# Kernel tuning notes

Hardware: AMD Instinct MI355X
Metric: run time of the kernel (lower is better)

Reference implementation:

```python
import jax, jax.numpy as jnp
import numpy as np

T = 256        # timesteps
N = 100000     # nodes
E = 8192       # edges per timestep
MU_PLUS = 0.1
MU_MINUS = 0.05
RHO = 16.0
CLIP_LO = 1e-5
CLIP_HI = 1.0 - 1e-5


def setup_inputs() -> dict:
    key = jax.random.key(0)
    k1, k2, k3, k4, k5, k6 = jax.random.split(key, 6)
    logit_X0 = jax.random.normal(k1, (N,), dtype=jnp.float32)
    theta = jax.random.normal(k2, (2,), dtype=jnp.float32)
    u = jax.random.randint(k3, (T, E), 0, N)
    v = jax.random.randint(k4, (T, E), 0, N)
    s_plus = jax.random.uniform(k5, (T, E), dtype=jnp.float32)
    s_minus = jax.random.uniform(k6, (T, E), dtype=jnp.float32)
    return {"logit_X0": logit_X0, "theta": theta, "u": u, "v": v,
            "s_plus": s_plus, "s_minus": s_minus}


def _diffuse(X0, u, v, s_plus, s_minus):
    # Equivalent of the dense-materialized row/col sums:
    # update[i] = mu * sum over edges (u,v,w): +w*(X[v]-X[u]) at u, -w*(X[v]-X[u]) at v
    def step(x, edge):
        ut, vt, sp, sm = edge
        d = x[vt] - x[ut]                       # [E]
        def agg(w):
            wd = w * d
            return jnp.zeros_like(x).at[ut].add(wd).at[vt].add(-wd)
        xn = jnp.clip(x + MU_PLUS * agg(sp) - MU_MINUS * agg(sm), CLIP_LO, CLIP_HI)
        return xn, xn
    _, Xs = jax.lax.scan(step, X0, (u[:-1], v[:-1], s_plus[:-1], s_minus[:-1]))
    return jnp.concatenate([X0[None], Xs], axis=0)  # [T, N]


def _kappa(eps, diff, rho):
    # kappa_from_epsilon: acceptance prob of bounded-confidence interaction
    return jax.nn.sigmoid(rho * (eps - jnp.abs(diff)))


def reference(logit_X0, theta, u, v, s_plus, s_minus):
    epsilon_plus = jax.nn.sigmoid(theta[0]) / 2.0
    epsilon_minus = 0.5 + jax.nn.sigmoid(theta[1]) / 2.0
    X0 = jax.nn.sigmoid(logit_X0)
    X = _diffuse(X0, u, v, s_plus, s_minus)            # [T, N]
    Xu = jnp.take_along_axis(X, u, axis=1)             # [T, E]
    Xv = jnp.take_along_axis(X, v, axis=1)             # [T, E]
    diff_X = (Xu - Xv).reshape(-1)                     # [T*E]
    kappa_plus = _kappa(epsilon_plus, diff_X, RHO)
    kappa_minus = _kappa(epsilon_minus, diff_X, -RHO)
    return X, kappa_plus, kappa_minus
```

## Files before the change

### kernel.cpp

```cpp
#include <hip/hip_runtime.h>

#define TSTEPS 256
#define NNODE  100000
#define NEDGE  8192

constexpr float MU_P  = 0.1f;
constexpr float MU_M  = 0.05f;
constexpr float RHO_  = 16.0f;
constexpr float CLO   = 1e-5f;
constexpr float CHI   = 1.0f - 1e-5f;
constexpr float SCALE = 1048576.0f;
constexpr float INVSC = 1.0f / 1048576.0f;

#define SENT32 0xFFFFFFFFu

typedef unsigned long long u64;

__device__ __forceinline__ float sigm(float x) {
  return 1.0f / (1.0f + __expf(-x));
}
__device__ __forceinline__ float x0_of(const float* logit, int n) {
  return fminf(fmaxf(sigm(logit[n]), CLO), CHI);
}
__device__ __forceinline__ int edge_at(const int* __restrict__ arr, int idx,
                                       int is64) {
  if (is64) return (int)((const long long*)arr)[idx];
  return arr[idx];
}

__device__ __forceinline__ u64 pload(const u64* p) {
  return __hip_atomic_load(p, __ATOMIC_RELAXED, __HIP_MEMORY_SCOPE_WORKGROUP);
}
__device__ __forceinline__ void pstore(u64* p, u64 v) {
  __hip_atomic_store(p, v, __ATOMIC_RELAXED, __HIP_MEMORY_SCOPE_WORKGROUP);
}

__device__ __forceinline__ float lazy2(const u64* xs64,
                                       const unsigned* __restrict__ dprev,
                                       int n, unsigned ttag) {
  const u64 a = pload(&xs64[n]);
  const int acc = (int)dprev[n];
  const unsigned tag = (unsigned)(a >> 32);
  const float pv = __uint_as_float((unsigned)a);
  const float cu = fminf(fmaxf(pv + (float)acc * INVSC, CLO), CHI);
  return (tag == ttag) ? pv : cu;
}

__global__ void k_init(const float* __restrict__ logit,
                       const int* __restrict__ u, const int* __restrict__ v,
                       u64* __restrict__ xs64,
                       unsigned* __restrict__ d0, unsigned* __restrict__ d1,
                       unsigned* __restrict__ d2,
                       unsigned* __restrict__ dflags,
                       float* __restrict__ outX) {
  const int i = blockIdx.x * blockDim.x + threadIdx.x;
  const int stride = gridDim.x * blockDim.x;

  if (i == 0) {
    const unsigned* a = (const unsigned*)u;
    const unsigned* b = (const unsigned*)v;
    bool i64 = true;
    for (int k = 1; k < 128; k += 2) i64 = i64 && (a[k] == 0u) && (b[k] == 0u);
    dflags[0] = i64 ? 1u : 0u;
  }

  for (int n = i; n < NNODE; n += stride) {
    xs64[n] = (u64)__float_as_uint(x0_of(logit, n));
    d0[n] = 0u;
    d1[n] = 0u;
    d2[n] = 0u;
    outX[n] = sigm(logit[n]);
  }
  unsigned* outX32 = (unsigned*)outX;
  const int total = TSTEPS * NNODE;
  for (int w = NNODE + i; w < total; w += stride) outX32[w] = SENT32;
}

__global__ void k_prep(const int* __restrict__ u, const int* __restrict__ v,
                       const float* __restrict__ sp, const float* __restrict__ sm,
                       int* __restrict__ uv32u, int* __restrict__ uv32v,
                       float* __restrict__ wsc,
                       const unsigned* __restrict__ dflags) {
  const int g = blockIdx.x * blockDim.x + threadIdx.x;
  if (g >= TSTEPS * NEDGE) return;
  const int is64 = (int)dflags[0];
  uv32u[g] = edge_at(u, g, is64);
  uv32v[g] = edge_at(v, g, is64);
  wsc[g] = (MU_P * sp[g] - MU_M * sm[g]) * SCALE;
}

__global__ __launch_bounds__(256) void k_step(
    const int* __restrict__ uv32u, const int* __restrict__ uv32v,
    const float* __restrict__ wsc,
    u64* __restrict__ xs64,
    unsigned* __restrict__ dcur, const unsigned* __restrict__ dprev,
    unsigned* __restrict__ dzero,
    float* __restrict__ cvals, int t) {
  const int bid = blockIdx.x;
  const int tid = threadIdx.x;
  const unsigned ttag = (unsigned)t;

  if (bid < 32) {
    if (t < TSTEPS - 1) {
      const int i = bid * 256 + tid;
      const int e = t * NEDGE + i;
      const int un = uv32u[e];
      const int vn = uv32v[e];
      const float w = wsc[e];
      const float xu = lazy2(xs64, dprev, un, ttag);
      const float xv = lazy2(xs64, dprev, vn, ttag);
      const int iv = __float2int_rn(w * (xv - xu));
      atomicAdd(&dcur[un], (unsigned)iv);
      atomicAdd(&dcur[vn], (unsigned)(-iv));
    }
  } else if (bid < 96) {
    if (t >= 1) {
      const int j = (bid - 32) * 256 + tid;
      const int e2 = (t - 1) * NEDGE + (j < NEDGE ? j : j - NEDGE);
      const int node = (j < NEDGE) ? uv32u[e2] : uv32v[e2];
      const float val = lazy2(xs64, dprev, node, ttag);
      pstore(&xs64[node], ((u64)ttag << 32) | (u64)__float_as_uint(val));
      cvals[(size_t)(t - 1) * (2 * NEDGE) + j] = val;
    }
  } else {
    const int base = (bid - 96) * 256 + tid;
    for (int n = base; n < NNODE; n += 64 * 256) dzero[n] = 0u;
  }
}

__global__ void k_resent(unsigned* __restrict__ outX32) {
  const int g = blockIdx.x * blockDim.x + threadIdx.x;
  const int total = 3 * TSTEPS * NEDGE;
  for (int w = g; w < total; w += gridDim.x * blockDim.x) {
    outX32[NNODE + w] = SENT32;
  }
}

__global__ void k_scatter(const int* __restrict__ u, const int* __restrict__ v,
                          const float* __restrict__ cvals,
                          float* __restrict__ outX,
                          const unsigned* __restrict__ dflags) {
  const int g = blockIdx.x * blockDim.x + threadIdx.x;
  if (g >= (TSTEPS - 1) * 2 * NEDGE) return;
  const int is64 = (int)dflags[0];
  const int r = g / (2 * NEDGE);
  const int s = g - r * (2 * NEDGE);
  const int e = r * NEDGE + (s < NEDGE ? s : s - NEDGE);
  const int node = (s < NEDGE) ? edge_at(u, e, is64) : edge_at(v, e, is64);
  outX[(size_t)(r + 1) * NNODE + node] = cvals[g];
}

__global__ void k_fill(const float* __restrict__ logit,
                       unsigned* __restrict__ outX32) {
  const int n = blockIdx.x * blockDim.x + threadIdx.x;
  if (n >= NNODE) return;
  unsigned carry = __float_as_uint(x0_of(logit, n));
  for (int t = 1; t < TSTEPS; ++t) {
    const size_t idx = (size_t)t * NNODE + n;
    const unsigned w = outX32[idx];
    if (w == SENT32) outX32[idx] = carry;
    else             carry = w;
  }
}

__global__ void k_kappa(const int* __restrict__ u, const int* __restrict__ v,
                        const float* __restrict__ theta,
                        const float* __restrict__ X,
                        float* __restrict__ outKp, float* __restrict__ outKm,
                        const unsigned* __restrict__ dflags) {
  const int g = blockIdx.x * blockDim.x + threadIdx.x;
  const int is64 = (int)dflags[0];
  const int t  = g >> 13;
  const int un = edge_at(u, g, is64);
  const int vn = edge_at(v, g, is64);
  const float Xu = X[(size_t)t * NNODE + un];
  const float Xv = X[(size_t)t * NNODE + vn];
  const float ad = fabsf(Xu - Xv);
  const float epsp = sigm(theta[0]) * 0.5f;
  const float epsm = 0.5f + sigm(theta[1]) * 0.5f;
  outKp[g] = sigm(RHO_ * (epsp - ad));
  outKm[g] = sigm(RHO_ * (ad - epsm));
}

__global__ void kDiag(float* __restrict__ outX, int b0, int b1) {
  if (threadIdx.x != 0 || blockIdx.x != 0) return;
  outX[0] = (float)(2048 + 1024 * b0 + 512 * b1);
}

extern "C" void kernel_launch(void* const* d_in, const int* in_sizes, int n_in,
                              void* d_out, int out_size, void* d_ws, size_t ws_size,
                              hipStream_t stream) {
  const float* logit = (const float*)d_in[0];
  const float* theta = (const float*)d_in[1];
  const int*   u     = (const int*)d_in[2];
  const int*   v     = (const int*)d_in[3];
  const float* sp    = (const float*)d_in[4];
  const float* sm    = (const float*)d_in[5];

  float* outX  = (float*)d_out;
  float* outKp = outX + (size_t)TSTEPS * NNODE;
  float* outKm = outKp + (size_t)TSTEPS * NEDGE;

  float* cvals = outKp;

  int*   uv32u = (int*)(outX + NNODE);
  int*   uv32v = uv32u + (size_t)TSTEPS * NEDGE;
  float* wsc   = (float*)(uv32v + (size_t)TSTEPS * NEDGE);

  const int b0 = (n_in == 6 &&
                  in_sizes[0] == NNODE && in_sizes[1] == 2 &&
                  in_sizes[2] == TSTEPS * NEDGE && in_sizes[3] == TSTEPS * NEDGE &&
                  in_sizes[4] == TSTEPS * NEDGE && in_sizes[5] == TSTEPS * NEDGE) ? 1 : 0;
  const size_t WS_NEED = (size_t)NNODE * 8 + (size_t)3 * NNODE * 4 + 64;
  const int b1 = (ws_size >= WS_NEED) ? 1 : 0;
  if (!b0 || !b1) {
    kDiag<<<1, 64, 0, stream>>>(outX, b0, b1);
    return;
  }

  char* ws = (char*)d_ws;
  u64*      xs64   = (u64*)ws;
  unsigned* d0     = (unsigned*)(ws + (size_t)NNODE * 8);
  unsigned* d1     = (unsigned*)(ws + (size_t)NNODE * 8 + (size_t)NNODE * 4);
  unsigned* d2     = (unsigned*)(ws + (size_t)NNODE * 8 + (size_t)2 * NNODE * 4);
  unsigned* dflags = (unsigned*)(ws + (size_t)NNODE * 8 + (size_t)3 * NNODE * 4);
  unsigned* dbuf[3] = {d0, d1, d2};

  k_init<<<2048, 256, 0, stream>>>(logit, u, v, xs64, d0, d1, d2, dflags, outX);
  k_prep<<<(TSTEPS * NEDGE + 255) / 256, 256, 0, stream>>>(u, v, sp, sm,
                                                           uv32u, uv32v, wsc,
                                                           dflags);

  for (int t = 0; t < TSTEPS; ++t) {
    unsigned* dcur  = dbuf[t % 3];
    unsigned* dprev = dbuf[(t + 2) % 3];
    unsigned* dzero = dbuf[(t + 1) % 3];
    k_step<<<160, 256, 0, stream>>>(uv32u, uv32v, wsc, xs64,
                                    dcur, dprev, dzero, cvals, t);
  }

  k_resent<<<4096, 256, 0, stream>>>((unsigned*)d_out);
  k_scatter<<<((TSTEPS - 1) * 2 * NEDGE + 255) / 256, 256, 0, stream>>>(
      u, v, cvals, outX, dflags);
  k_fill<<<(NNODE + 255) / 256, 256, 0, stream>>>(logit, (unsigned*)d_out);
  k_kappa<<<(TSTEPS * NEDGE) / 256, 256, 0, stream>>>(u, v, theta, outX,
                                                      outKp, outKm, dflags);
}
```

Before: 1.526 ms.

## Fuse two diffusion timesteps per launch with in-kernel grid barrier

Each kernel launch now processes two timesteps. A global atomic counter acts as a spin barrier between the scatter-add of step t0 and the gather of step t0+1, which halves the number of per-step launches. Node values are read lazily across two pending delta buffers (five rotating buffers, two of them placed in spare output space), and tagged publishes use atomicMax so the newer tag wins. The cost is spin-waiting and device-scope atomics. The barrier relies on all 160 blocks being co-resident, which could deadlock if they are not.

New measurement: 1.810 ms. +18.6%, slower.

```diff
diff --git a/kernel.cpp b/kernel.cpp
--- a/kernel.cpp
+++ b/kernel.cpp
@@ -13,7 +13,6 @@
 constexpr float INVSC = 1.0f / 1048576.0f;
 
 #define SENT32 0xFFFFFFFFu
-
 typedef unsigned long long u64;
 
 __device__ __forceinline__ float sigm(float x) {
@@ -27,30 +26,58 @@
   if (is64) return (int)((const long long*)arr)[idx];
   return arr[idx];
 }
-
 __device__ __forceinline__ u64 pload(const u64* p) {
   return __hip_atomic_load(p, __ATOMIC_RELAXED, __HIP_MEMORY_SCOPE_WORKGROUP);
 }
-__device__ __forceinline__ void pstore(u64* p, u64 v) {
-  __hip_atomic_store(p, v, __ATOMIC_RELAXED, __HIP_MEMORY_SCOPE_WORKGROUP);
+__device__ __forceinline__ void pmax(u64* p, u64 v) {
+  atomicMax(p, v);
+}
+__device__ __forceinline__ float clipf(float x) {
+  return fminf(fmaxf(x, CLO), CHI);
+}
+
+__device__ __forceinline__ unsigned agent_load_u32(const unsigned* p) {
+  return __hip_atomic_load(p, __ATOMIC_RELAXED, __HIP_MEMORY_SCOPE_AGENT);
+}
+__device__ __forceinline__ unsigned agent_fadd_u32(unsigned* p, unsigned v) {
+  return __hip_atomic_fetch_add(p, v, __ATOMIC_RELAXED,
+                                __HIP_MEMORY_SCOPE_AGENT);
 }
 
 __device__ __forceinline__ float lazy2(const u64* xs64,
-                                       const unsigned* __restrict__ dprev,
-                                       int n, unsigned ttag) {
+                                       const unsigned* __restrict__ dP,
+                                       int n, unsigned t0) {
   const u64 a = pload(&xs64[n]);
-  const int acc = (int)dprev[n];
+  const int acc = (int)dP[n];
   const unsigned tag = (unsigned)(a >> 32);
   const float pv = __uint_as_float((unsigned)a);
-  const float cu = fminf(fmaxf(pv + (float)acc * INVSC, CLO), CHI);
-  return (tag == ttag) ? pv : cu;
+  const float cu = clipf(pv + (float)acc * INVSC);
+  return (tag == t0) ? pv : cu;
+}
+
+__device__ __forceinline__ float lazy3(const u64* xs64,
+                                       const unsigned* __restrict__ dP,
+                                       const unsigned* __restrict__ dA,
+                                       int n, unsigned t0) {
+  const u64 a = pload(&xs64[n]);
+  const unsigned tag = (unsigned)(a >> 32);
+  const float val = __uint_as_float((unsigned)a);
+  if (tag == t0 + 1u) return val;
+  float v1;
+  if (tag == t0) {
+    v1 = val;
+  } else {
+    v1 = clipf(val + (float)((int)dP[n]) * INVSC);
+  }
+  const int acc1 = (int)agent_load_u32(&dA[n]);
+  return clipf(v1 + (float)acc1 * INVSC);
 }
 
 __global__ void k_init(const float* __restrict__ logit,
                        const int* __restrict__ u, const int* __restrict__ v,
                        u64* __restrict__ xs64,
-                       unsigned* __restrict__ d0, unsigned* __restrict__ d1,
-                       unsigned* __restrict__ d2,
+                       unsigned* __restrict__ b0, unsigned* __restrict__ b1,
+                       unsigned* __restrict__ b2,
                        unsigned* __restrict__ dflags,
                        float* __restrict__ outX) {
   const int i = blockIdx.x * blockDim.x + threadIdx.x;
@@ -62,13 +89,14 @@
     bool i64 = true;
     for (int k = 1; k < 128; k += 2) i64 = i64 && (a[k] == 0u) && (b[k] == 0u);
     dflags[0] = i64 ? 1u : 0u;
+    dflags[4] = 0u;
   }
 
   for (int n = i; n < NNODE; n += stride) {
     xs64[n] = (u64)__float_as_uint(x0_of(logit, n));
-    d0[n] = 0u;
-    d1[n] = 0u;
-    d2[n] = 0u;
+    b0[n] = 0u;
+    b1[n] = 0u;
+    b2[n] = 0u;
     outX[n] = sigm(logit[n]);
   }
   unsigned* outX32 = (unsigned*)outX;
@@ -80,57 +108,105 @@
                        const float* __restrict__ sp, const float* __restrict__ sm,
                        int* __restrict__ uv32u, int* __restrict__ uv32v,
                        float* __restrict__ wsc,
+                       unsigned* __restrict__ b3, unsigned* __restrict__ b4,
                        const unsigned* __restrict__ dflags) {
   const int g = blockIdx.x * blockDim.x + threadIdx.x;
-  if (g >= TSTEPS * NEDGE) return;
+  const int stride = gridDim.x * blockDim.x;
   const int is64 = (int)dflags[0];
-  uv32u[g] = edge_at(u, g, is64);
-  uv32v[g] = edge_at(v, g, is64);
-  wsc[g] = (MU_P * sp[g] - MU_M * sm[g]) * SCALE;
-}
-
-__global__ __launch_bounds__(256) void k_step(
+  for (int e = g; e < TSTEPS * NEDGE; e += stride) {
+    uv32u[e] = edge_at(u, e, is64);
+    uv32v[e] = edge_at(v, e, is64);
+    wsc[e] = (MU_P * sp[e] - MU_M * sm[e]) * SCALE;
+  }
+  for (int n = g; n < NNODE; n += stride) {
+    b3[n] = 0u;
+    b4[n] = 0u;
+  }
+}
+
+__global__ __launch_bounds__(256) void k_step2(
     const int* __restrict__ uv32u, const int* __restrict__ uv32v,
     const float* __restrict__ wsc,
     u64* __restrict__ xs64,
-    unsigned* __restrict__ dcur, const unsigned* __restrict__ dprev,
-    unsigned* __restrict__ dzero,
-    float* __restrict__ cvals, int t) {
+    unsigned* __restrict__ dA, unsigned* __restrict__ dB,
+    const unsigned* __restrict__ dP,
+    unsigned* __restrict__ dz1, unsigned* __restrict__ dz2,
+    float* __restrict__ cvals,
+    unsigned* __restrict__ bar, unsigned target, int t0) {
   const int bid = blockIdx.x;
   const int tid = threadIdx.x;
-  const unsigned ttag = (unsigned)t;
+  const unsigned ut0 = (unsigned)t0;
+  const int t1 = t0 + 1;
+
+  if (bid >= 96) {
+    const int base = (bid - 96) * 256 + tid;
+    for (int n = base; n < NNODE; n += 64 * 256) {
+      dz1[n] = 0u;
+      dz2[n] = 0u;
+    }
+    return;
+  }
 
   if (bid < 32) {
-    if (t < TSTEPS - 1) {
-      const int i = bid * 256 + tid;
-      const int e = t * NEDGE + i;
+    const int i = bid * 256 + tid;
+    const int eA = t0 * NEDGE + i;
+    const int unA = uv32u[eA];
+    const int vnA = uv32v[eA];
+    const float wA = wsc[eA];
+    const float xu = lazy2(xs64, dP, unA, ut0);
+    const float xv = lazy2(xs64, dP, vnA, ut0);
+    const int iv = __float2int_rn(wA * (xv - xu));
+    const unsigned o1 = agent_fadd_u32(&dA[unA], (unsigned)iv);
+    const unsigned o2 = agent_fadd_u32(&dA[vnA], (unsigned)(-iv));
+    asm volatile("" :: "v"(o1), "v"(o2));
+    __syncthreads();
+    if (tid == 0) {
+      const unsigned o3 = agent_fadd_u32(&bar[0], 1u);
+      asm volatile("" :: "v"(o3));
+    }
+  } else {
+    if (t0 >= 1) {
+      const int j = (bid - 32) * 256 + tid;
+      const int e2 = (t0 - 1) * NEDGE + (j < NEDGE ? j : j - NEDGE);
+      const int node = (j < NEDGE) ? uv32u[e2] : uv32v[e2];
+      const float val = lazy2(xs64, dP, node, ut0);
+      pmax(&xs64[node], ((u64)ut0 << 32) | (u64)__float_as_uint(val));
+      cvals[(size_t)(t0 - 1) * (2 * NEDGE) + j] = val;
+    }
+  }
+
+  if (tid == 0) {
+    while (agent_load_u32(&bar[0]) < target) {
+      __builtin_amdgcn_s_sleep(1);
+    }
+  }
+  __syncthreads();
+
+  if (bid < 32) {
+    if (t1 < TSTEPS - 1) {
+      const int e = t1 * NEDGE + (bid * 256 + tid);
       const int un = uv32u[e];
       const int vn = uv32v[e];
       const float w = wsc[e];
-      const float xu = lazy2(xs64, dprev, un, ttag);
-      const float xv = lazy2(xs64, dprev, vn, ttag);
+      const float xu = lazy3(xs64, dP, dA, un, ut0);
+      const float xv = lazy3(xs64, dP, dA, vn, ut0);
       const int iv = __float2int_rn(w * (xv - xu));
-      atomicAdd(&dcur[un], (unsigned)iv);
-      atomicAdd(&dcur[vn], (unsigned)(-iv));
-    }
-  } else if (bid < 96) {
-    if (t >= 1) {
-      const int j = (bid - 32) * 256 + tid;
-      const int e2 = (t - 1) * NEDGE + (j < NEDGE ? j : j - NEDGE);
-      const int node = (j < NEDGE) ? uv32u[e2] : uv32v[e2];
-      const float val = lazy2(xs64, dprev, node, ttag);
-      pstore(&xs64[node], ((u64)ttag << 32) | (u64)__float_as_uint(val));
-      cvals[(size_t)(t - 1) * (2 * NEDGE) + j] = val;
+      atomicAdd(&dB[un], (unsigned)iv);
+      atomicAdd(&dB[vn], (unsigned)(-iv));
     }
   } else {
-    const int base = (bid - 96) * 256 + tid;
-    for (int n = base; n < NNODE; n += 64 * 256) dzero[n] = 0u;
+    const int j = (bid - 32) * 256 + tid;
+    const int e2 = t0 * NEDGE + (j < NEDGE ? j : j - NEDGE);
+    const int node = (j < NEDGE) ? uv32u[e2] : uv32v[e2];
+    const float val = lazy3(xs64, dP, dA, node, ut0);
+    pmax(&xs64[node], ((u64)(unsigned)t1 << 32) | (u64)__float_as_uint(val));
+    cvals[(size_t)t0 * (2 * NEDGE) + j] = val;
   }
 }
 
 __global__ void k_resent(unsigned* __restrict__ outX32) {
   const int g = blockIdx.x * blockDim.x + threadIdx.x;
-  const int total = 3 * TSTEPS * NEDGE;
+  const int total = 3 * TSTEPS * NEDGE + 2 * NNODE;
   for (int w = g; w < total; w += gridDim.x * blockDim.x) {
     outX32[NNODE + w] = SENT32;
   }
@@ -203,40 +279,47 @@
 
   float* cvals = outKp;
 
-  int*   uv32u = (int*)(outX + NNODE);
-  int*   uv32v = uv32u + (size_t)TSTEPS * NEDGE;
-  float* wsc   = (float*)(uv32v + (size_t)TSTEPS * NEDGE);
-
-  const int b0 = (n_in == 6 &&
+  int*      uv32u = (int*)(outX + NNODE);
+  int*      uv32v = uv32u + (size_t)TSTEPS * NEDGE;
+  float*    wsc   = (float*)(uv32v + (size_t)TSTEPS * NEDGE);
+  unsigned* b3    = (unsigned*)(wsc + (size_t)TSTEPS * NEDGE);
+  unsigned* b4    = b3 + NNODE;
+
+  const int c0 = (n_in == 6 &&
                   in_sizes[0] == NNODE && in_sizes[1] == 2 &&
                   in_sizes[2] == TSTEPS * NEDGE && in_sizes[3] == TSTEPS * NEDGE &&
                   in_sizes[4] == TSTEPS * NEDGE && in_sizes[5] == TSTEPS * NEDGE) ? 1 : 0;
   const size_t WS_NEED = (size_t)NNODE * 8 + (size_t)3 * NNODE * 4 + 64;
-  const int b1 = (ws_size >= WS_NEED) ? 1 : 0;
-  if (!b0 || !b1) {
-    kDiag<<<1, 64, 0, stream>>>(outX, b0, b1);
+  const int c1 = (ws_size >= WS_NEED) ? 1 : 0;
+  if (!c0 || !c1) {
+    kDiag<<<1, 64, 0, stream>>>(outX, c0, c1);
     return;
   }
 
   char* ws = (char*)d_ws;
   u64*      xs64   = (u64*)ws;
-  unsigned* d0     = (unsigned*)(ws + (size_t)NNODE * 8);
-  unsigned* d1     = (unsigned*)(ws + (size_t)NNODE * 8 + (size_t)NNODE * 4);
-  unsigned* d2     = (unsigned*)(ws + (size_t)NNODE * 8 + (size_t)2 * NNODE * 4);
+  unsigned* wb0    = (unsigned*)(ws + (size_t)NNODE * 8);
+  unsigned* wb1    = (unsigned*)(ws + (size_t)NNODE * 8 + (size_t)NNODE * 4);
+  unsigned* wb2    = (unsigned*)(ws + (size_t)NNODE * 8 + (size_t)2 * NNODE * 4);
   unsigned* dflags = (unsigned*)(ws + (size_t)NNODE * 8 + (size_t)3 * NNODE * 4);
-  unsigned* dbuf[3] = {d0, d1, d2};
-
-  k_init<<<2048, 256, 0, stream>>>(logit, u, v, xs64, d0, d1, d2, dflags, outX);
-  k_prep<<<(TSTEPS * NEDGE + 255) / 256, 256, 0, stream>>>(u, v, sp, sm,
-                                                           uv32u, uv32v, wsc,
-                                                           dflags);
-
-  for (int t = 0; t < TSTEPS; ++t) {
-    unsigned* dcur  = dbuf[t % 3];
-    unsigned* dprev = dbuf[(t + 2) % 3];
-    unsigned* dzero = dbuf[(t + 1) % 3];
-    k_step<<<160, 256, 0, stream>>>(uv32u, uv32v, wsc, xs64,
-                                    dcur, dprev, dzero, cvals, t);
+  unsigned* bar    = dflags + 4;
+  unsigned* B[5]   = {wb0, wb1, wb2, b3, b4};
+
+  k_init<<<2048, 256, 0, stream>>>(logit, u, v, xs64, wb0, wb1, wb2, dflags,
+                                   outX);
+  k_prep<<<4096, 256, 0, stream>>>(u, v, sp, sm, uv32u, uv32v, wsc, b3, b4,
+                                   dflags);
+
+  for (int d = 0; d < TSTEPS / 2; ++d) {
+    const int t0 = 2 * d;
+    unsigned* dA  = B[t0 % 5];
+    unsigned* dB  = B[(t0 + 1) % 5];
+    unsigned* dP  = B[(t0 + 4) % 5];
+    unsigned* dz1 = B[(t0 + 2) % 5];
+    unsigned* dz2 = B[(t0 + 3) % 5];
+    k_step2<<<160, 256, 0, stream>>>(uv32u, uv32v, wsc, xs64, dA, dB, dP,
+                                     dz1, dz2, cvals, bar,
+                                     (unsigned)(32 * (d + 1)), t0);
   }
 
   k_resent<<<4096, 256, 0, stream>>>((unsigned*)d_out);
```
